# Performance work log

Hardware: AMD Instinct MI355X
Metric: run time of the kernel (lower is better)

The kernel has to match this reference:

```python
import jax, jax.numpy as jnp
import numpy as np

EPS = 1e-5
GRID_SIZE = 5
SPLINE_ORDER = 3
WINDOW = 16  # local_window_size hardcoded in Block


def _make_grid(in_features):
    h = 2.0 / GRID_SIZE  # grid_range [-1, 1]
    g = (np.arange(-SPLINE_ORDER, GRID_SIZE + SPLINE_ORDER + 1) * h - 1.0).astype(np.float32)
    return jnp.asarray(np.tile(g[None, :], (in_features, 1)))  # (in, 12)


def layer_norm(x, g, b):
    mu = jnp.mean(x, axis=-1, keepdims=True)
    var = jnp.var(x, axis=-1, keepdims=True)
    return (x - mu) * jax.lax.rsqrt(var + EPS) * g + b


def b_splines(x, grid):
    # x: (M, in) -> (M, in, GRID_SIZE + SPLINE_ORDER)
    xe = x[..., None]
    bases = ((xe >= grid[:, :-1]) & (xe < grid[:, 1:])).astype(x.dtype)
    for k in range(1, SPLINE_ORDER + 1):
        bases = ((xe - grid[:, : -(k + 1)]) / (grid[:, k:-1] - grid[:, : -(k + 1)]) * bases[..., :-1]
                 + (grid[:, k + 1:] - xe) / (grid[:, k + 1:] - grid[:, 1:-k]) * bases[..., 1:])
    return bases


def kan_linear(x, base_w, spline_w, spline_scaler, grid):
    base = jax.nn.silu(x) @ base_w.T  # (M, out)
    sw = spline_w * spline_scaler[..., None]  # (out, in, K)
    spline = jnp.einsum('mik,oik->mo', b_splines(x, grid), sw)
    return base + spline


def conv1d(h, w, b):
    # h: (B, C, T), w: (O, I, 3) or (O, I, k); padding 'same' for k=3 pad=1
    pad = (w.shape[-1] - 1) // 2
    out = jax.lax.conv_general_dilated(h, w, window_strides=(1,), padding=[(pad, pad)],
                                       dimension_numbers=('NCH', 'OIH', 'NCH'))
    return out + b[None, :, None]


def setup_inputs() -> dict:
    key = jax.random.key(0)
    ks = jax.random.split(key, 20)
    B, N, C = 8, 1024, 48
    H = 8
    hid = 24
    K = GRID_SIZE + SPLINE_ORDER
    s = 0.05
    inp = {
        'x': jax.random.normal(ks[0], (B, N, C), dtype=jnp.float32),
        'g1': jnp.ones((C,), jnp.float32), 'b1': jnp.zeros((C,), jnp.float32),
        'w_qkv': jax.random.normal(ks[1], (3 * C, C), jnp.float32) * s,
        'w_proj': jax.random.normal(ks[2], (C, C), jnp.float32) * s,
        'b_proj': jnp.zeros((C,), jnp.float32),
        'g2': jnp.ones((C,), jnp.float32), 'b2': jnp.zeros((C,), jnp.float32),
        'bw1': jax.random.normal(ks[3], (hid, C), jnp.float32) * s,
        'sw1': jax.random.normal(ks[4], (hid, C, K), jnp.float32) * s,
        'ss1': jnp.ones((hid, C), jnp.float32),
        'bw2': jax.random.normal(ks[5], (C, hid), jnp.float32) * s,
        'sw2': jax.random.normal(ks[6], (C, hid, K), jnp.float32) * s,
        'ss2': jnp.ones((C, hid), jnp.float32),
        'conv1_w': jax.random.normal(ks[7], (128, C, 3), jnp.float32) * s,
        'conv1_b': jnp.zeros((128,), jnp.float32),
        'conv3_w': jax.random.normal(ks[8], (C, 128, 3), jnp.float32) * s,
        'conv3_b': jnp.zeros((C,), jnp.float32),
        'sc': jnp.asarray(0.1, jnp.float32),
    }
    return inp


def reference(x, g1, b1, w_qkv, w_proj, b_proj, g2, b2,
              bw1, sw1, ss1, bw2, sw2, ss2,
              conv1_w, conv1_b, conv3_w, conv3_b, sc):
    B, N, C = x.shape
    H = 8
    hd = C // H
    scale = hd ** -0.5

    n1 = layer_norm(x, g1, b1)
    qkv = (n1 @ w_qkv.T).reshape(B, N, 3, H, hd)
    q, k, v = (qkv[:, :, 0].transpose(0, 2, 1, 3),
               qkv[:, :, 1].transpose(0, 2, 1, 3),
               qkv[:, :, 2].transpose(0, 2, 1, 3))  # (B, H, N, hd)

    # global attention
    attn_global = jax.nn.softmax(jnp.einsum('bhqd,bhkd->bhqk', q, k) * scale, axis=-1)
    x_global = jnp.einsum('bhqk,bhkd->bhqd', attn_global, v)
    x_global = x_global.transpose(0, 2, 1, 3).reshape(B, N, C)

    # local (non-overlapping window) attention, vectorized over windows
    W = WINDOW
    nw = N // W
    qw = q.reshape(B, H, nw, W, hd)
    kw = k.reshape(B, H, nw, W, hd)
    vw = v.reshape(B, H, nw, W, hd)
    attn_local = jax.nn.softmax(jnp.einsum('bhnqd,bhnkd->bhnqk', qw, kw) * scale, axis=-1)
    x_local = jnp.einsum('bhnqk,bhnkd->bhnqd', attn_local, vw)
    x_local = x_local.reshape(B, H, N, hd).transpose(0, 2, 1, 3).reshape(B, N, C)

    attn_out = (x_global + x_local) @ w_proj.T + b_proj
    x1 = x + attn_out

    # KAN MLP on norm2(x1), flattened tokens
    n2 = layer_norm(x1, g2, b2).reshape(-1, C)
    grid1 = _make_grid(C)
    grid2 = _make_grid(bw1.shape[0])
    kan_h = kan_linear(n2, bw1, sw1, ss1, grid1)
    kan_o = kan_linear(kan_h, bw2, sw2, ss2, grid2).reshape(B, N, C)
    x2 = x1 + kan_o

    # conv residual path on the original input
    h = x.transpose(0, 2, 1)  # (B, C, N)
    h = conv1d(h, conv1_w, conv1_b)
    h = conv1d(h, conv3_w, conv3_b)
    h = h.transpose(0, 2, 1)  # (B, N, C)
    h = layer_norm(h, g1, b1)  # Block reuses norm1 here

    out = sc * h + x2
    return (out, attn_global)
```

## Files before the change

kernel.cpp:

```cpp
#include <hip/hip_runtime.h>

static constexpr int B = 8, N = 1024, C = 48, H = 8, HD = 6, NT = B * N;
static constexpr int QKVO = 3 * C;
static constexpr int HID = 24, KB = 8;
static constexpr int C1 = 128;

#define DEVFN __device__ __forceinline__

DEVFN float wsum(float v) {
#pragma unroll
  for (int m = 32; m; m >>= 1) v += __shfl_xor(v, m, 64);
  return v;
}
DEVFN float wmax(float v) {
#pragma unroll
  for (int m = 32; m; m >>= 1) v = fmaxf(v, __shfl_xor(v, m, 64));
  return v;
}
DEVFN float gsum16(float v) {
#pragma unroll
  for (int m = 8; m; m >>= 1) v += __shfl_xor(v, m, 16);
  return v;
}
DEVFN float gmax16(float v) {
#pragma unroll
  for (int m = 8; m; m >>= 1) v = fmaxf(v, __shfl_xor(v, m, 16));
  return v;
}

DEVFN void bspline8(float x, float* bs) {
  float b[11];
#pragma unroll
  for (int j = 0; j < 11; ++j) {
    float gj = -2.2f + 0.4f * j;
    float gj1 = -2.2f + 0.4f * (j + 1);
    b[j] = (x >= gj && x < gj1) ? 1.0f : 0.0f;
  }
#pragma unroll
  for (int j = 0; j < 10; ++j) {
    float gj = -2.2f + 0.4f * j;
    b[j] = (x - gj) * 2.5f * b[j] + ((gj + 0.8f) - x) * 2.5f * b[j + 1];
  }
#pragma unroll
  for (int j = 0; j < 9; ++j) {
    float gj = -2.2f + 0.4f * j;
    b[j] = (x - gj) * 1.25f * b[j] + ((gj + 1.2f) - x) * 1.25f * b[j + 1];
  }
#pragma unroll
  for (int j = 0; j < 8; ++j) {
    float gj = -2.2f + 0.4f * j;
    bs[j] = (x - gj) * (1.0f / 1.2f) * b[j] + ((gj + 1.6f) - x) * (1.0f / 1.2f) * b[j + 1];
  }
}

__global__ __launch_bounds__(256) void k_ln_qkv(
    const float* __restrict__ x, const float* __restrict__ g1, const float* __restrict__ b1,
    const float* __restrict__ wqkv, float* __restrict__ q, float* __restrict__ k,
    float* __restrict__ v) {
  __shared__ float wl[QKVO * 49];
  __shared__ float nb[4][C];
  int tid = threadIdx.x;
  for (int e = tid; e < QKVO * C; e += 256) wl[(e / C) * 49 + (e % C)] = wqkv[e];
  int wave = tid >> 6, lane = tid & 63;
  int tok = blockIdx.x * 4 + wave;
  const float* xr = x + tok * C;
  float xv = (lane < C) ? xr[lane] : 0.f;
  float s = wsum(xv), s2 = wsum(xv * xv);
  float mean = s * (1.f / C);
  float var = s2 * (1.f / C) - mean * mean;
  float rstd = rsqrtf(var + 1e-5f);
  if (lane < C) nb[wave][lane] = (xv - mean) * rstd * g1[lane] + b1[lane];
  __syncthreads();
  int b = tok >> 10, n = tok & 1023;
#pragma unroll
  for (int r = 0; r < 3; ++r) {
    int o = lane + (r << 6);
    if (o < QKVO) {
      float acc = 0.f;
#pragma unroll
      for (int i = 0; i < C; ++i) acc += nb[wave][i] * wl[o * 49 + i];
      int ssel = o / C;
      int rem = o - ssel * C;
      int hh = rem / HD;
      int d = rem - hh * HD;
      float* dst = ssel == 0 ? q : (ssel == 1 ? k : v);
      dst[((b * H + hh) * N + n) * HD + d] = acc;
    }
  }
}

__global__ __launch_bounds__(256) void k_gattn(
    const float* __restrict__ q, const float* __restrict__ k, const float* __restrict__ v,
    float* __restrict__ attn, float* __restrict__ xgl) {
  __shared__ float2 kt[3][N];
  __shared__ float2 vt[3][N];
  __shared__ float ob[64][6];
  int tid = threadIdx.x;
  int bh = blockIdx.x >> 4;
  int rb = blockIdx.x & 15;
  const float* kg = k + bh * N * HD;
  const float* vg = v + bh * N * HD;
  float* ktf = (float*)kt;
  float* vtf = (float*)vt;
  for (int e = tid; e < N * HD; e += 256) {
    int kp = e / 6, d = e - kp * 6;
    int a = (d >> 1) * 2048 + (kp << 1) + (d & 1);
    ktf[a] = kg[e];
    vtf[a] = vg[e];
  }
  __syncthreads();
  int wave = tid >> 6, lane = tid & 63;
  const float scl = 0.40824829046386301637f;
  int b = bh >> 3, hh = bh & 7;
  int r0 = rb * 64 + wave * 16;
#pragma unroll 2
  for (int rr = 0; rr < 16; ++rr) {
    int qrow = r0 + rr;
    const float2* qp = (const float2*)(q + (bh * N + qrow) * HD);
    float2 q0 = qp[0], q1 = qp[1], q2 = qp[2];
    float sv[16];
    float mx = -1e30f;
#pragma unroll
    for (int it = 0; it < 16; ++it) {
      int kp = lane + (it << 6);
      float2 a0 = kt[0][kp], a1 = kt[1][kp], a2 = kt[2][kp];
      float dp = q0.x * a0.x + q0.y * a0.y + q1.x * a1.x + q1.y * a1.y + q2.x * a2.x + q2.y * a2.y;
      sv[it] = dp * scl;
      mx = fmaxf(mx, sv[it]);
    }
    mx = wmax(mx);
    float sum = 0.f;
#pragma unroll
    for (int it = 0; it < 16; ++it) {
      sv[it] = __expf(sv[it] - mx);
      sum += sv[it];
    }
    sum = wsum(sum);
    float inv = 1.f / sum;
    float a0 = 0, a1 = 0, a2 = 0, a3 = 0, a4 = 0, a5 = 0;
    float* arow = attn + (size_t)(bh * N + qrow) * N;
#pragma unroll
    for (int it = 0; it < 16; ++it) {
      int kp = lane + (it << 6);
      float p = sv[it];
      __builtin_nontemporal_store(p * inv, arow + kp);
      float2 v0 = vt[0][kp], v1 = vt[1][kp], v2 = vt[2][kp];
      a0 += p * v0.x; a1 += p * v0.y; a2 += p * v1.x;
      a3 += p * v1.y; a4 += p * v2.x; a5 += p * v2.y;
    }
    a0 = wsum(a0) * inv; a1 = wsum(a1) * inv; a2 = wsum(a2) * inv;
    a3 = wsum(a3) * inv; a4 = wsum(a4) * inv; a5 = wsum(a5) * inv;
    if (lane == 0) {
      int li = wave * 16 + rr;
      ob[li][0] = a0; ob[li][1] = a1; ob[li][2] = a2;
      ob[li][3] = a3; ob[li][4] = a4; ob[li][5] = a5;
    }
  }
  int n0 = r0;
  int kk = lane & 15, g = lane >> 4;
  float kv[6], vv[6];
#pragma unroll
  for (int d = 0; d < 6; ++d) {
    int a = (d >> 1) * 2048 + ((n0 + kk) << 1) + (d & 1);
    kv[d] = ktf[a];
    vv[d] = vtf[a];
  }
#pragma unroll
  for (int pass = 0; pass < 4; ++pass) {
    int qr = n0 + pass * 4 + g;
    const float* qp = q + (bh * N + qr) * HD;
    float s = 0.f;
#pragma unroll
    for (int d = 0; d < 6; ++d) s += qp[d] * kv[d];
    s *= scl;
    float mx = gmax16(s);
    float p = __expf(s - mx);
    float sum = gsum16(p);
    float inv = 1.f / sum;
    float o[6];
#pragma unroll
    for (int d = 0; d < 6; ++d) o[d] = gsum16(p * vv[d]) * inv;
    if (kk == 0) {
      int li = wave * 16 + pass * 4 + g;
      float* dst = xgl + (size_t)(b * N + qr) * C + hh * HD;
#pragma unroll
      for (int d = 0; d < 6; ++d) dst[d] = ob[li][d] + o[d];
    }
  }
}

__global__ __launch_bounds__(512) void k_mlp(
    const float* __restrict__ x, const float* __restrict__ xgl,
    const float* __restrict__ wp, const float* __restrict__ bp,
    const float* __restrict__ g2, const float* __restrict__ b2,
    const float* __restrict__ bw1, const float* __restrict__ sw1, const float* __restrict__ ss1,
    const float* __restrict__ bw2, const float* __restrict__ sw2, const float* __restrict__ ss2,
    float* __restrict__ x2) {
  __shared__ float wpl[C * 49];
  __shared__ float bw1t[C * 25];
  __shared__ float ss1t[C * 25];
  __shared__ float sw1t[C * KB * 25];
  __shared__ float bw2t[HID * 49];
  __shared__ float ss2t[HID * 49];
  __shared__ float sw2t[HID * KB * 49];
  __shared__ float abuf[8][2][C];
  __shared__ float sil1[8][2][C];
  __shared__ float bas1[8][2][C][KB];
  __shared__ float sil2[8][2][HID];
  __shared__ float bas2[8][2][HID][KB];
  int tid = threadIdx.x;
  for (int e = tid; e < C * C; e += 512) wpl[(e / C) * 49 + (e % C)] = wp[e];
  for (int e = tid; e < HID * C; e += 512) {
    int o = e / C, i = e - o * C;
    bw1t[i * 25 + o] = bw1[e];
    ss1t[i * 25 + o] = ss1[e];
  }
  for (int e = tid; e < HID * C * KB; e += 512) {
    int o = e / (C * KB), r = e - o * (C * KB);
    sw1t[r * 25 + o] = sw1[e];
  }
  for (int e = tid; e < C * HID; e += 512) {
    int o = e / HID, i = e - o * HID;
    bw2t[i * 49 + o] = bw2[e];
    ss2t[i * 49 + o] = ss2[e];
  }
  for (int e = tid; e < C * HID * KB; e += 512) {
    int o = e / (HID * KB), r = e - o * (HID * KB);
    sw2t[r * 49 + o] = sw2[e];
  }
  __syncthreads();
  int wave = tid >> 6, lane = tid & 63;
  int tok0 = blockIdx.x * 16 + wave * 2;
  float x1v[2];
#pragma unroll
  for (int tt = 0; tt < 2; ++tt) {
    int tok = tok0 + tt;
    float acc = 0.f, xin = 0.f;
    if (lane < C) {
      abuf[wave][tt][lane] = xgl[tok * C + lane];
      xin = x[tok * C + lane];
    }
    if (lane < C) {
      acc = bp[lane];
#pragma unroll
      for (int i = 0; i < C; ++i) acc += abuf[wave][tt][i] * wpl[lane * 49 + i];
    }
    float xv = (lane < C) ? xin + acc : 0.f;
    x1v[tt] = xv;
    float s = wsum(xv), s2 = wsum(xv * xv);
    float mean = s * (1.f / C), var = s2 * (1.f / C) - mean * mean;
    float rstd = rsqrtf(var + 1e-5f);
    if (lane < C) {
      float n2v = (xv - mean) * rstd * g2[lane] + b2[lane];
      sil1[wave][tt][lane] = n2v / (1.f + __expf(-n2v));
      float bs[KB];
      bspline8(n2v, bs);
#pragma unroll
      for (int kk = 0; kk < KB; ++kk) bas1[wave][tt][lane][kk] = bs[kk];
    }
  }
  int o = lane & 31, hf = lane >> 5;
  float h0 = 0.f, h1 = 0.f;
  if (o < HID) {
#pragma unroll 4
    for (int ii = 0; ii < 24; ++ii) {
      int i = hf * 24 + ii;
      float bwv = bw1t[i * 25 + o], ssv = ss1t[i * 25 + o];
      float sp0 = 0.f, sp1 = 0.f;
#pragma unroll
      for (int kk = 0; kk < KB; ++kk) {
        float w = sw1t[(i * KB + kk) * 25 + o];
        sp0 += bas1[wave][0][i][kk] * w;
        sp1 += bas1[wave][1][i][kk] * w;
      }
      h0 += sil1[wave][0][i] * bwv + ssv * sp0;
      h1 += sil1[wave][1][i] * bwv + ssv * sp1;
    }
  }
  h0 += __shfl_xor(h0, 32, 64);
  h1 += __shfl_xor(h1, 32, 64);
  if (lane < HID) {
    float hv[2] = {h0, h1};
#pragma unroll
    for (int tt = 0; tt < 2; ++tt) {
      sil2[wave][tt][lane] = hv[tt] / (1.f + __expf(-hv[tt]));
      float bs[KB];
      bspline8(hv[tt], bs);
#pragma unroll
      for (int kk = 0; kk < KB; ++kk) bas2[wave][tt][lane][kk] = bs[kk];
    }
  }
  if (lane < C) {
    float a0 = 0.f, a1 = 0.f;
#pragma unroll 4
    for (int i = 0; i < HID; ++i) {
      float bwv = bw2t[i * 49 + lane], ssv = ss2t[i * 49 + lane];
      float sp0 = 0.f, sp1 = 0.f;
#pragma unroll
      for (int kk = 0; kk < KB; ++kk) {
        float w = sw2t[(i * KB + kk) * 49 + lane];
        sp0 += bas2[wave][0][i][kk] * w;
        sp1 += bas2[wave][1][i][kk] * w;
      }
      a0 += sil2[wave][0][i] * bwv + ssv * sp0;
      a1 += sil2[wave][1][i] * bwv + ssv * sp1;
    }
    x2[(size_t)tok0 * C + lane] = x1v[0] + a0;
    x2[(size_t)(tok0 + 1) * C + lane] = x1v[1] + a1;
  }
}

__global__ __launch_bounds__(256) void k_conv1(
    const float* __restrict__ x, const float* __restrict__ w1, const float* __restrict__ bc1,
    float* __restrict__ h1) {
  __shared__ float wt[72 * C1];
  __shared__ float xr[18 * C];
  int tid = threadIdx.x;
  int b = blockIdx.x >> 6;
  int t0 = (blockIdx.x & 63) << 4;
  for (int e = tid; e < 18 * C; e += 256) {
    int r = e / C, c = e - r * C;
    int n = t0 - 1 + r;
    xr[e] = (n >= 0 && n < N) ? x[(b * N + n) * C + c] : 0.f;
  }
  int wave = tid >> 6, lane = tid & 63;
  int tb = wave << 2;
  float acc0[4] = {0, 0, 0, 0}, acc1[4] = {0, 0, 0, 0};
  for (int hf = 0; hf < 2; ++hf) {
    __syncthreads();
    for (int e = tid; e < 72 * C1; e += 256) {
      int i3 = e >> 7, o = e & 127;
      int ii = i3 / 3, dk = i3 - ii * 3;
      wt[e] = w1[(o * C + hf * 24 + ii) * 3 + dk];
    }
    __syncthreads();
#pragma unroll 4
    for (int ii = 0; ii < 24; ++ii) {
      float xv[6];
#pragma unroll
      for (int j = 0; j < 6; ++j) xv[j] = xr[(tb + j) * C + hf * 24 + ii];
#pragma unroll
      for (int dk = 0; dk < 3; ++dk) {
        float w0 = wt[(ii * 3 + dk) * C1 + lane];
        float w1v = wt[(ii * 3 + dk) * C1 + 64 + lane];
#pragma unroll
        for (int tt = 0; tt < 4; ++tt) {
          float xi = xv[tt + dk];
          acc0[tt] += xi * w0;
          acc1[tt] += xi * w1v;
        }
      }
    }
  }
  float bb0 = bc1[lane], bb1 = bc1[64 + lane];
#pragma unroll
  for (int tt = 0; tt < 4; ++tt) {
    int n = t0 + tb + tt;
    h1[(b * N + n) * C1 + lane] = acc0[tt] + bb0;
    h1[(b * N + n) * C1 + 64 + lane] = acc1[tt] + bb1;
  }
}

__global__ __launch_bounds__(256) void k_conv2out(
    const float* __restrict__ h1, const float* __restrict__ w3, const float* __restrict__ bc3,
    const float* __restrict__ g1, const float* __restrict__ b1,
    const float* __restrict__ x2, const float* __restrict__ scp,
    float* __restrict__ out) {
  __shared__ float wt[192 * C + 16];
  __shared__ float hr[18 * C1];
  int tid = threadIdx.x;
  int b = blockIdx.x >> 6;
  int t0 = (blockIdx.x & 63) << 4;
  for (int e = tid; e < 18 * C1; e += 256) {
    int r = e >> 7, c = e & 127;
    int n = t0 - 1 + r;
    hr[e] = (n >= 0 && n < N) ? h1[(b * N + n) * C1 + c] : 0.f;
  }
  int wave = tid >> 6, lane = tid & 63;
  int tb = wave << 2;
  float acc[4] = {0, 0, 0, 0};
  for (int hf = 0; hf < 2; ++hf) {
    __syncthreads();
    for (int e = tid; e < 192 * C; e += 256) {
      int i3 = e / C, c = e - i3 * C;
      int ii = i3 / 3, dk = i3 - ii * 3;
      wt[e] = w3[(c * C1 + hf * 64 + ii) * 3 + dk];
    }
    __syncthreads();
#pragma unroll 4
    for (int ii = 0; ii < 64; ++ii) {
      float xv[6];
#pragma unroll
      for (int j = 0; j < 6; ++j) xv[j] = hr[(tb + j) * C1 + hf * 64 + ii];
#pragma unroll
      for (int dk = 0; dk < 3; ++dk) {
        float w = wt[(ii * 3 + dk) * C + lane];
#pragma unroll
        for (int tt = 0; tt < 4; ++tt) acc[tt] += xv[tt + dk] * w;
      }
    }
  }
  float sc0 = scp[0];
#pragma unroll
  for (int tt = 0; tt < 4; ++tt) {
    int n = t0 + tb + tt;
    float val = (lane < C) ? acc[tt] + bc3[lane] : 0.f;
    float s = wsum(val), s2 = wsum(val * val);
    float mean = s * (1.f / C), var = s2 * (1.f / C) - mean * mean;
    float rstd = rsqrtf(var + 1e-5f);
    if (lane < C) {
      float hn = (val - mean) * rstd * g1[lane] + b1[lane];
      out[(b * N + n) * C + lane] = sc0 * hn + x2[(size_t)(b * N + n) * C + lane];
    }
  }
}

extern "C" void kernel_launch(void* const* d_in, const int* in_sizes, int n_in,
                              void* d_out, int out_size, void* d_ws, size_t ws_size,
                              hipStream_t stream) {
  (void)in_sizes; (void)n_in; (void)out_size; (void)ws_size;
  const float* x    = (const float*)d_in[0];
  const float* g1   = (const float*)d_in[1];
  const float* b1   = (const float*)d_in[2];
  const float* wqkv = (const float*)d_in[3];
  const float* wp   = (const float*)d_in[4];
  const float* bp   = (const float*)d_in[5];
  const float* g2   = (const float*)d_in[6];
  const float* b2   = (const float*)d_in[7];
  const float* bw1  = (const float*)d_in[8];
  const float* sw1  = (const float*)d_in[9];
  const float* ss1  = (const float*)d_in[10];
  const float* bw2  = (const float*)d_in[11];
  const float* sw2  = (const float*)d_in[12];
  const float* ss2  = (const float*)d_in[13];
  const float* w1   = (const float*)d_in[14];
  const float* bc1  = (const float*)d_in[15];
  const float* w3   = (const float*)d_in[16];
  const float* bc3  = (const float*)d_in[17];
  const float* scp  = (const float*)d_in[18];

  float* out  = (float*)d_out;
  float* attn = out + (size_t)NT * C;

  float* ws   = (float*)d_ws;
  float* q    = ws;
  float* k    = ws + 393216;
  float* v    = ws + 786432;
  float* xgl  = ws + 1179648;
  float* x2   = ws + 1572864;
  float* h1   = ws + 1966080;

  k_ln_qkv<<<NT / 4, 256, 0, stream>>>(x, g1, b1, wqkv, q, k, v);
  k_gattn<<<B * H * 16, 256, 0, stream>>>(q, k, v, attn, xgl);
  k_mlp<<<NT / 16, 512, 0, stream>>>(x, xgl, wp, bp, g2, b2,
                                     bw1, sw1, ss1, bw2, sw2, ss2, x2);
  k_conv1<<<512, 256, 0, stream>>>(x, w1, bc1, h1);
  k_conv2out<<<512, 256, 0, stream>>>(h1, w3, bc3, g1, b1, x2, scp, out);
}
```

Before: 504.0 us.

## Process multiple query rows per wave in global attention and two tokens in QKV

```diff
diff --git a/kernel.cpp b/kernel.cpp
--- a/kernel.cpp
+++ b/kernel.cpp
@@ -58,38 +58,46 @@
     const float* __restrict__ wqkv, float* __restrict__ q, float* __restrict__ k,
     float* __restrict__ v) {
   __shared__ float wl[QKVO * 49];
-  __shared__ float nb[4][C];
+  __shared__ float nb[4][2][C];
   int tid = threadIdx.x;
   for (int e = tid; e < QKVO * C; e += 256) wl[(e / C) * 49 + (e % C)] = wqkv[e];
   int wave = tid >> 6, lane = tid & 63;
-  int tok = blockIdx.x * 4 + wave;
-  const float* xr = x + tok * C;
-  float xv = (lane < C) ? xr[lane] : 0.f;
-  float s = wsum(xv), s2 = wsum(xv * xv);
-  float mean = s * (1.f / C);
-  float var = s2 * (1.f / C) - mean * mean;
-  float rstd = rsqrtf(var + 1e-5f);
-  if (lane < C) nb[wave][lane] = (xv - mean) * rstd * g1[lane] + b1[lane];
+  int tok0 = blockIdx.x * 8 + wave * 2;
+#pragma unroll
+  for (int tt = 0; tt < 2; ++tt) {
+    const float* xr = x + (tok0 + tt) * C;
+    float xv = (lane < C) ? xr[lane] : 0.f;
+    float s = wsum(xv), s2 = wsum(xv * xv);
+    float mean = s * (1.f / C);
+    float var = s2 * (1.f / C) - mean * mean;
+    float rstd = rsqrtf(var + 1e-5f);
+    if (lane < C) nb[wave][tt][lane] = (xv - mean) * rstd * g1[lane] + b1[lane];
+  }
   __syncthreads();
-  int b = tok >> 10, n = tok & 1023;
+  int b = tok0 >> 10, n0 = tok0 & 1023;
 #pragma unroll
   for (int r = 0; r < 3; ++r) {
     int o = lane + (r << 6);
     if (o < QKVO) {
-      float acc = 0.f;
-#pragma unroll
-      for (int i = 0; i < C; ++i) acc += nb[wave][i] * wl[o * 49 + i];
+      float a0 = 0.f, a1 = 0.f;
+#pragma unroll
+      for (int i = 0; i < C; ++i) {
+        float w = wl[o * 49 + i];
+        a0 += nb[wave][0][i] * w;
+        a1 += nb[wave][1][i] * w;
+      }
       int ssel = o / C;
       int rem = o - ssel * C;
       int hh = rem / HD;
       int d = rem - hh * HD;
       float* dst = ssel == 0 ? q : (ssel == 1 ? k : v);
-      dst[((b * H + hh) * N + n) * HD + d] = acc;
-    }
-  }
-}
-
-__global__ __launch_bounds__(256) void k_gattn(
+      dst[((b * H + hh) * N + n0) * HD + d] = a0;
+      dst[((b * H + hh) * N + n0 + 1) * HD + d] = a1;
+    }
+  }
+}
+
+__global__ __launch_bounds__(256, 3) void k_gattn(
     const float* __restrict__ q, const float* __restrict__ k, const float* __restrict__ v,
     float* __restrict__ attn, float* __restrict__ xgl) {
   __shared__ float2 kt[3][N];
@@ -113,47 +121,73 @@
   const float scl = 0.40824829046386301637f;
   int b = bh >> 3, hh = bh & 7;
   int r0 = rb * 64 + wave * 16;
-#pragma unroll 2
-  for (int rr = 0; rr < 16; ++rr) {
-    int qrow = r0 + rr;
-    const float2* qp = (const float2*)(q + (bh * N + qrow) * HD);
-    float2 q0 = qp[0], q1 = qp[1], q2 = qp[2];
-    float sv[16];
-    float mx = -1e30f;
+#pragma unroll 1
+  for (int t4 = 0; t4 < 4; ++t4) {
+    int qbase = r0 + t4 * 4;
+    float2 qr[4][3];
+#pragma unroll
+    for (int rj = 0; rj < 4; ++rj) {
+      const float2* qp = (const float2*)(q + (bh * N + qbase + rj) * HD);
+      qr[rj][0] = qp[0]; qr[rj][1] = qp[1]; qr[rj][2] = qp[2];
+    }
+    float sv[4][16];
+    float mx[4] = {-1e30f, -1e30f, -1e30f, -1e30f};
 #pragma unroll
     for (int it = 0; it < 16; ++it) {
       int kp = lane + (it << 6);
-      float2 a0 = kt[0][kp], a1 = kt[1][kp], a2 = kt[2][kp];
-      float dp = q0.x * a0.x + q0.y * a0.y + q1.x * a1.x + q1.y * a1.y + q2.x * a2.x + q2.y * a2.y;
-      sv[it] = dp * scl;
-      mx = fmaxf(mx, sv[it]);
-    }
-    mx = wmax(mx);
-    float sum = 0.f;
+      float2 k0 = kt[0][kp], k1 = kt[1][kp], k2 = kt[2][kp];
+#pragma unroll
+      for (int rj = 0; rj < 4; ++rj) {
+        float dp = qr[rj][0].x * k0.x + qr[rj][0].y * k0.y + qr[rj][1].x * k1.x +
+                   qr[rj][1].y * k1.y + qr[rj][2].x * k2.x + qr[rj][2].y * k2.y;
+        sv[rj][it] = dp * scl;
+        mx[rj] = fmaxf(mx[rj], sv[rj][it]);
+      }
+    }
+#pragma unroll
+    for (int rj = 0; rj < 4; ++rj) mx[rj] = wmax(mx[rj]);
+    float sum[4] = {0.f, 0.f, 0.f, 0.f};
 #pragma unroll
     for (int it = 0; it < 16; ++it) {
-      sv[it] = __expf(sv[it] - mx);
-      sum += sv[it];
-    }
-    sum = wsum(sum);
-    float inv = 1.f / sum;
-    float a0 = 0, a1 = 0, a2 = 0, a3 = 0, a4 = 0, a5 = 0;
-    float* arow = attn + (size_t)(bh * N + qrow) * N;
+#pragma unroll
+      for (int rj = 0; rj < 4; ++rj) {
+        sv[rj][it] = __expf(sv[rj][it] - mx[rj]);
+        sum[rj] += sv[rj][it];
+      }
+    }
+#pragma unroll
+    for (int rj = 0; rj < 4; ++rj) sum[rj] = 1.f / wsum(sum[rj]);
+#pragma unroll
+    for (int it = 0; it < 16; ++it) {
+#pragma unroll
+      for (int rj = 0; rj < 4; ++rj) sv[rj][it] *= sum[rj];
+    }
+    float acc[4][6];
+#pragma unroll
+    for (int rj = 0; rj < 4; ++rj)
+#pragma unroll
+      for (int d = 0; d < 6; ++d) acc[rj][d] = 0.f;
 #pragma unroll
     for (int it = 0; it < 16; ++it) {
       int kp = lane + (it << 6);
-      float p = sv[it];
-      __builtin_nontemporal_store(p * inv, arow + kp);
       float2 v0 = vt[0][kp], v1 = vt[1][kp], v2 = vt[2][kp];
-      a0 += p * v0.x; a1 += p * v0.y; a2 += p * v1.x;
-      a3 += p * v1.y; a4 += p * v2.x; a5 += p * v2.y;
-    }
-    a0 = wsum(a0) * inv; a1 = wsum(a1) * inv; a2 = wsum(a2) * inv;
-    a3 = wsum(a3) * inv; a4 = wsum(a4) * inv; a5 = wsum(a5) * inv;
-    if (lane == 0) {
-      int li = wave * 16 + rr;
-      ob[li][0] = a0; ob[li][1] = a1; ob[li][2] = a2;
-      ob[li][3] = a3; ob[li][4] = a4; ob[li][5] = a5;
+#pragma unroll
+      for (int rj = 0; rj < 4; ++rj) {
+        float p = sv[rj][it];
+        __builtin_nontemporal_store(p, attn + (size_t)(bh * N + qbase + rj) * N + kp);
+        acc[rj][0] += p * v0.x; acc[rj][1] += p * v0.y; acc[rj][2] += p * v1.x;
+        acc[rj][3] += p * v1.y; acc[rj][4] += p * v2.x; acc[rj][5] += p * v2.y;
+      }
+    }
+#pragma unroll
+    for (int rj = 0; rj < 4; ++rj) {
+#pragma unroll
+      for (int d = 0; d < 6; ++d) acc[rj][d] = wsum(acc[rj][d]);
+      if (lane == 0) {
+        int li = wave * 16 + t4 * 4 + rj;
+#pragma unroll
+        for (int d = 0; d < 6; ++d) ob[li][d] = acc[rj][d];
+      }
     }
   }
   int n0 = r0;
@@ -167,22 +201,22 @@
   }
 #pragma unroll
   for (int pass = 0; pass < 4; ++pass) {
-    int qr = n0 + pass * 4 + g;
-    const float* qp = q + (bh * N + qr) * HD;
+    int qr2 = n0 + pass * 4 + g;
+    const float* qp = q + (bh * N + qr2) * HD;
     float s = 0.f;
 #pragma unroll
     for (int d = 0; d < 6; ++d) s += qp[d] * kv[d];
     s *= scl;
-    float mx = gmax16(s);
-    float p = __expf(s - mx);
-    float sum = gsum16(p);
-    float inv = 1.f / sum;
+    float mx2 = gmax16(s);
+    float p = __expf(s - mx2);
+    float sum2 = gsum16(p);
+    float inv = 1.f / sum2;
     float o[6];
 #pragma unroll
     for (int d = 0; d < 6; ++d) o[d] = gsum16(p * vv[d]) * inv;
     if (kk == 0) {
       int li = wave * 16 + pass * 4 + g;
-      float* dst = xgl + (size_t)(b * N + qr) * C + hh * HD;
+      float* dst = xgl + (size_t)(b * N + qr2) * C + hh * HD;
 #pragma unroll
       for (int d = 0; d < 6; ++d) dst[d] = ob[li][d] + o[d];
     }
@@ -450,7 +484,7 @@
   float* x2   = ws + 1572864;
   float* h1   = ws + 1966080;
 
-  k_ln_qkv<<<NT / 4, 256, 0, stream>>>(x, g1, b1, wqkv, q, k, v);
+  k_ln_qkv<<<NT / 8, 256, 0, stream>>>(x, g1, b1, wqkv, q, k, v);
   k_gattn<<<B * H * 16, 256, 0, stream>>>(q, k, v, attn, xgl);
   k_mlp<<<NT / 16, 512, 0, stream>>>(x, xgl, wp, bp, g2, b2,
                                      bw1, sw1, ss1, bw2, sw2, ss2, x2);
```

New measurement: 561.0 us. +11.3%, slower.
